# Performance work log

Hardware: AMD Instinct MI355X
Metric: run time of the kernel (lower is better)

The kernel has to match this reference:

```python
import jax, jax.numpy as jnp
import numpy as np

S = 2048          # sequence length (single prefill sequence)
HID = 4096        # hidden_size
NH, NKV, HD = 32, 8, 128   # q heads, kv heads, head_dim
THETA = 10000.0
SCALE = HD ** -0.5


def setup_inputs() -> dict:
    key = jax.random.key(0)
    k1, k2, k3 = jax.random.split(key, 3)
    hidden_states = jax.random.normal(k1, (S, HID), jnp.float32)
    positions = jnp.arange(S, dtype=jnp.int32)
    W_qkv = jax.random.normal(k2, (HID, (NH + 2 * NKV) * HD), jnp.float32) * 0.02
    W_o = jax.random.normal(k3, (NH * HD, HID), jnp.float32) * 0.02
    return {"hidden_states": hidden_states, "positions": positions,
            "W_qkv": W_qkv, "W_o": W_o}


def _rope(x, positions):
    # x: [T, H, HD]; neox-style RoPE (rotate halves, is_neox_style=True)
    half = HD // 2
    inv_freq = 1.0 / (THETA ** (jnp.arange(half, dtype=jnp.float32) / half))
    freqs = positions.astype(jnp.float32)[:, None] * inv_freq[None, :]  # [T, half]
    cos = jnp.cos(freqs)[:, None, :]
    sin = jnp.sin(freqs)[:, None, :]
    x1, x2 = x[..., :half], x[..., half:]
    return jnp.concatenate([x1 * cos - x2 * sin, x2 * cos + x1 * sin], axis=-1)


def reference(hidden_states, positions, W_qkv, W_o):
    # fused QKV projection then split (q_size = NH*HD, kv_size = NKV*HD)
    qkv = hidden_states @ W_qkv                      # [S, (NH+2*NKV)*HD]
    q, k, v = jnp.split(qkv, [NH * HD, NH * HD + NKV * HD], axis=1)
    q = _rope(q.reshape(S, NH, HD), positions)       # [S, NH, HD]
    k = _rope(k.reshape(S, NKV, HD), positions)      # [S, NKV, HD]
    v = v.reshape(S, NKV, HD)
    # GQA: broadcast kv heads to query heads
    rep = NH // NKV
    k = jnp.repeat(k, rep, axis=1)                   # [S, NH, HD]
    v = jnp.repeat(v, rep, axis=1)
    scores = jnp.einsum('qhd,khd->hqk', q, k) * SCALE  # [NH, S, S]
    causal = jnp.tril(jnp.ones((S, S), dtype=bool))
    scores = jnp.where(causal[None], scores, jnp.finfo(scores.dtype).min)
    attn = jax.nn.softmax(scores, axis=-1)
    out = jnp.einsum('hqk,khd->qhd', attn, v).reshape(S, NH * HD)
    return out @ W_o                                 # [S, HID]
```

## Files before the change

kernel.cpp:

```cpp
#include <hip/hip_runtime.h>
#include <math.h>

#define S_LEN 2048
#define HID 4096
#define NH 32
#define NKV 8
#define HD 128
#define QKV_N ((NH + 2*NKV) * HD)
#define NQK (NH + NKV)
static __device__ __constant__ const float SCALE_F = 0.08838834764831845f;

typedef __bf16 bf16x8 __attribute__((ext_vector_type(8)));
typedef __bf16 bf16x4 __attribute__((ext_vector_type(4)));
typedef float  f32x4  __attribute__((ext_vector_type(4)));

#define GLD_LDS(gptr, lptr) \
  __builtin_amdgcn_global_load_lds( \
      (const __attribute__((address_space(1))) uint32_t*)(gptr), \
      (__attribute__((address_space(3))) uint32_t*)(lptr), 16, 0, 0)

__global__ void cast_bf16_kernel(const float4* __restrict__ in, __bf16* __restrict__ out, int n4) {
  int i = blockIdx.x * blockDim.x + threadIdx.x;
  if (i >= n4) return;
  float4 v = in[i];
  bf16x4 o = { (__bf16)v.x, (__bf16)v.y, (__bf16)v.z, (__bf16)v.w };
  *(bf16x4*)(out + (size_t)i * 4) = o;
}

__global__ void transpose_cast_kernel(const float* __restrict__ in, __bf16* __restrict__ out,
                                      int R, int C) {
  __shared__ float tile[32][33];
  int bx = blockIdx.x * 32;
  int by = blockIdx.y * 32;
  int tx = threadIdx.x, ty = threadIdx.y;
  for (int i = 0; i < 32; i += 8)
    tile[ty + i][tx] = in[(size_t)(by + ty + i) * C + bx + tx];
  __syncthreads();
  for (int i = 0; i < 32; i += 8)
    out[(size_t)(bx + ty + i) * R + by + tx] = (__bf16)tile[tx][ty + i];
}

__global__ void transpose_v_kernel(const __bf16* __restrict__ qkv, __bf16* __restrict__ Vt) {
  __shared__ __bf16 tile[32][33];
  int kvh = blockIdx.z;
  int sb = blockIdx.x * 32;
  int db = blockIdx.y * 32;
  int tx = threadIdx.x, ty = threadIdx.y;
  const __bf16* src = qkv + (size_t)(NH + NKV) * HD + (size_t)kvh * HD;
  for (int i = 0; i < 32; i += 8)
    tile[ty + i][tx] = src[(size_t)(sb + ty + i) * QKV_N + db + tx];
  __syncthreads();
  for (int i = 0; i < 32; i += 8)
    Vt[((size_t)kvh * HD + db + ty + i) * S_LEN + sb + tx] = tile[tx][ty + i];
}

__global__ void rope_kernel(const __bf16* __restrict__ qkv, const int* __restrict__ pos,
                            __bf16* __restrict__ Qr, __bf16* __restrict__ Kr) {
  int idx = blockIdx.x * blockDim.x + threadIdx.x;
  int half = idx & 63;
  int t = idx >> 6;
  int hh = t % NQK;
  int s = t / NQK;
  if (s >= S_LEN) return;
  float p = (float)pos[s];
  float inv_freq = exp2f((float)half * -0.2076205059304601f);
  float ang = p * inv_freq;
  float cs = cosf(ang), sn = sinf(ang);
  const __bf16* src; __bf16* dst;
  if (hh < NH) {
    src = qkv + (size_t)s * QKV_N + (size_t)hh * HD;
    dst = Qr + ((size_t)s * NH + hh) * HD;
  } else {
    int kh = hh - NH;
    src = qkv + (size_t)s * QKV_N + (size_t)NH * HD + (size_t)kh * HD;
    dst = Kr + ((size_t)s * NKV + kh) * HD;
  }
  float x1 = (float)src[half], x2 = (float)src[half + 64];
  dst[half]      = (__bf16)(x1 * cs - x2 * sn);
  dst[half + 64] = (__bf16)(x2 * cs + x1 * sn);
}

template <typename OutT>
__global__ __launch_bounds__(512, 2) void gemm8p_kernel(const __bf16* __restrict__ A,
                                                        const __bf16* __restrict__ Bt,
                                                        OutT* __restrict__ C,
                                                        int M, int N, int K) {
  __shared__ __align__(16) __bf16 sA[2][2][256 * 32];
  __shared__ __align__(16) __bf16 sB[2][2][256 * 32];
  const int tid = threadIdx.x;
  const int lane = tid & 63;
  const int wave = tid >> 6;
  const int quad = lane >> 4;
  const int l16 = lane & 15;
  const int wm = (wave >> 2) * 128;
  const int wn = (wave & 3) * 64;
  const size_t bm = (size_t)blockIdx.y * 256;
  const size_t bn = (size_t)blockIdx.x * 256;
  const int NT = K >> 6;
  const int rsw = (l16 >> 1) & 3;

  f32x4 acc[8][4] = {};
  bf16x8 aR[4], bR[4];

#define STAGE(gbase, rowbase, tau, h, dst) do {                                   \
    size_t kof_ = (size_t)((tau) % NT) * 64 + (h) * 32;                           \
    _Pragma("unroll")                                                             \
    for (int it_ = 0; it_ < 2; ++it_) {                                           \
      int c_ = it_ * 512 + tid;                                                   \
      int row_ = c_ >> 2, ch_ = c_ & 3;                                           \
      int chL_ = ch_ ^ ((row_ >> 1) & 3);                                         \
      GLD_LDS(&(gbase)[((rowbase) + row_) * (size_t)K + kof_ + chL_ * 8],         \
              &(dst)[c_ * 8]);                                                    \
    }                                                                             \
  } while (0)

#define LOADB(bf, kk) do {                                                        \
    _Pragma("unroll")                                                             \
    for (int j_ = 0; j_ < 4; ++j_)                                                \
      bR[j_] = *(const bf16x8*)&sB[bf][kk][(wn + j_ * 16 + l16) * 32 +            \
                                           ((quad ^ rsw) * 8)];                   \
  } while (0)

#define LOADA(bf, kk, ih) do {                                                    \
    _Pragma("unroll")                                                             \
    for (int i_ = 0; i_ < 4; ++i_)                                                \
      aR[i_] = *(const bf16x8*)&sA[bf][kk][(wm + ((ih) * 4 + i_) * 16 + l16) * 32 \
                                           + ((quad ^ rsw) * 8)];                 \
  } while (0)

#define MFMA16(ih) do {                                                           \
    __builtin_amdgcn_s_setprio(1);                                                \
    _Pragma("unroll")                                                             \
    for (int i_ = 0; i_ < 4; ++i_)                                                \
      _Pragma("unroll")                                                           \
      for (int j_ = 0; j_ < 4; ++j_)                                              \
        acc[(ih) * 4 + i_][j_] = __builtin_amdgcn_mfma_f32_16x16x32_bf16(         \
            aR[i_], bR[j_], acc[(ih) * 4 + i_][j_], 0, 0, 0);                     \
    __builtin_amdgcn_s_setprio(0);                                                \
  } while (0)

#define BAR() __builtin_amdgcn_s_barrier()
#define VMCNT4() asm volatile("s_waitcnt vmcnt(4)" ::: "memory")

  STAGE(A,  bm, 0, 0, sA[0][0]);
  STAGE(Bt, bn, 0, 0, sB[0][0]);
  STAGE(A,  bm, 0, 1, sA[0][1]);
  STAGE(Bt, bn, 0, 1, sB[0][1]);
  STAGE(A,  bm, 1, 0, sA[1][0]);
  STAGE(Bt, bn, 1, 0, sB[1][0]);
  VMCNT4();
  BAR();

  for (int u = 0; u < (NT >> 1); ++u) {
    const int t0 = 2 * u;
    LOADB(0, 0); LOADA(0, 0, 0);
    STAGE(A, bm, t0 + 1, 1, sA[1][1]);
    BAR();
    MFMA16(0);
    BAR();
    LOADA(0, 0, 1);
    STAGE(Bt, bn, t0 + 1, 1, sB[1][1]);
    BAR();
    MFMA16(1);
    BAR();
    LOADB(0, 1); LOADA(0, 1, 0);
    STAGE(A, bm, t0 + 2, 0, sA[0][0]);
    BAR();
    MFMA16(0);
    BAR();
    LOADA(0, 1, 1);
    STAGE(Bt, bn, t0 + 2, 0, sB[0][0]);
    BAR();
    MFMA16(1);
    VMCNT4();
    BAR();
    LOADB(1, 0); LOADA(1, 0, 0);
    STAGE(A, bm, t0 + 2, 1, sA[0][1]);
    BAR();
    MFMA16(0);
    BAR();
    LOADA(1, 0, 1);
    STAGE(Bt, bn, t0 + 2, 1, sB[0][1]);
    BAR();
    MFMA16(1);
    BAR();
    LOADB(1, 1); LOADA(1, 1, 0);
    STAGE(A, bm, t0 + 3, 0, sA[1][0]);
    BAR();
    MFMA16(0);
    BAR();
    LOADA(1, 1, 1);
    STAGE(Bt, bn, t0 + 3, 0, sB[1][0]);
    BAR();
    MFMA16(1);
    VMCNT4();
    BAR();
  }

  asm volatile("s_waitcnt vmcnt(0)" ::: "memory");

  #pragma unroll
  for (int i = 0; i < 8; ++i)
    #pragma unroll
    for (int j = 0; j < 4; ++j)
      #pragma unroll
      for (int r = 0; r < 4; ++r) {
        size_t row = bm + wm + i * 16 + quad * 4 + r;
        size_t col = bn + wn + j * 16 + l16;
        C[row * (size_t)N + col] = (OutT)acc[i][j][r];
      }

#undef STAGE
#undef LOADB
#undef LOADA
#undef MFMA16
#undef BAR
#undef VMCNT4
}

__global__ __launch_bounds__(256, 2) void attn_kernel(const __bf16* __restrict__ Qr,
                                                      const __bf16* __restrict__ Kr,
                                                      const __bf16* __restrict__ Vt,
                                                      __bf16* __restrict__ O) {
  __shared__ __align__(16) char smem[73728];
  __bf16* Ps = (__bf16*)(smem + 65536);

  const int bid = blockIdx.x;
  const int h = bid & (NH - 1);
  const int qb = (S_LEN / 64 - 1) - (bid >> 5);
  const int kvh = h >> 2;
  const int tid = threadIdx.x;
  const int lane = tid & 63, wave = tid >> 6;
  const int quad = lane >> 4, l16 = lane & 15;
  const int sw = l16 & 7;
  const int q0 = qb * 64;

#define STAGE_KV(kbase, bufv) do {                                                 \
    char* kd_ = smem + (bufv) * 16384;                                             \
    char* vd_ = smem + 32768 + (bufv) * 16384;                                     \
    _Pragma("unroll")                                                              \
    for (int pass_ = 0; pass_ < 4; ++pass_) {                                      \
      int c_ = pass_ * 256 + tid;                                                  \
      int row_ = c_ >> 4, ch_ = c_ & 15;                                           \
      int chs_ = ch_ ^ (row_ & 7);                                                 \
      GLD_LDS(&Kr[(size_t)((kbase) + row_) * (NKV * HD) + (size_t)kvh * HD + chs_ * 8], \
              kd_ + c_ * 16);                                                      \
    }                                                                              \
    _Pragma("unroll")                                                              \
    for (int pass_ = 0; pass_ < 4; ++pass_) {                                      \
      int c_ = pass_ * 256 + tid;                                                  \
      int d_ = c_ >> 3, ch_ = c_ & 7;                                              \
      int chs_ = ch_ ^ (d_ & 7);                                                   \
      GLD_LDS(&Vt[((size_t)kvh * HD + d_) * S_LEN + (kbase) + chs_ * 8],           \
              vd_ + c_ * 16);                                                      \
    }                                                                              \
  } while (0)

  bf16x8 qf[4];
  {
    const __bf16* qp = Qr + (size_t)(q0 + wave * 16 + l16) * (NH * HD) + (size_t)h * HD + quad * 8;
    for (int kk = 0; kk < 4; ++kk) qf[kk] = *(const bf16x8*)(qp + kk * 32);
  }
  f32x4 oacc[8] = {};
  float m2 = -INFINITY, l_i = 0.0f;
  const float C2 = SCALE_F * 1.4426950408889634f;

  int buf = 0;
  STAGE_KV(0, 0);
  for (int kb = 0; kb <= q0; kb += 64) {
    __syncthreads();
    if (kb + 64 <= q0) STAGE_KV(kb + 64, buf ^ 1);

    const __bf16* Ks = (const __bf16*)(smem + buf * 16384);
    const __bf16* Vs = (const __bf16*)(smem + 32768 + buf * 16384);

    f32x4 sc[4] = {};
    __builtin_amdgcn_s_setprio(1);
    for (int jt = 0; jt < 4; ++jt)
      for (int kk = 0; kk < 4; ++kk) {
        bf16x8 kf = *(const bf16x8*)&Ks[(jt * 16 + l16) * 128 + ((kk * 4 + quad) ^ sw) * 8];
        sc[jt] = __builtin_amdgcn_mfma_f32_16x16x32_bf16(kf, qf[kk], sc[jt], 0, 0, 0);
      }
    __builtin_amdgcn_s_setprio(0);

    float s[16];
    for (int jt = 0; jt < 4; ++jt)
      for (int r = 0; r < 4; ++r) s[jt * 4 + r] = sc[jt][r];
    if (kb == q0) {
      int qloc = wave * 16 + l16;
      for (int jt = 0; jt < 4; ++jt)
        for (int r = 0; r < 4; ++r)
          if (jt * 16 + quad * 4 + r > qloc) s[jt * 4 + r] = -INFINITY;
    }
    float mx = s[0];
    for (int i = 1; i < 16; ++i) mx = fmaxf(mx, s[i]);
    mx = fmaxf(mx, __shfl_xor(mx, 16, 64));
    mx = fmaxf(mx, __shfl_xor(mx, 32, 64));
    float m2new = fmaxf(m2, mx * C2);
    float alpha = exp2f(m2 - m2new);
    float pv[16], sum = 0.0f;
    for (int i = 0; i < 16; ++i) { pv[i] = exp2f(fmaf(s[i], C2, -m2new)); sum += pv[i]; }
    sum += __shfl_xor(sum, 16, 64);
    sum += __shfl_xor(sum, 32, 64);
    l_i = l_i * alpha + sum;
    m2 = m2new;
    for (int dt = 0; dt < 8; ++dt) oacc[dt] *= alpha;

    __bf16* pw = Ps + wave * 1024 + l16 * 64;
    for (int jt = 0; jt < 4; ++jt) {
      bf16x4 pk = { (__bf16)pv[jt*4+0], (__bf16)pv[jt*4+1], (__bf16)pv[jt*4+2], (__bf16)pv[jt*4+3] };
      int chunk = jt * 2 + (quad >> 1);
      *(bf16x4*)&pw[((chunk ^ sw) * 8) + (quad & 1) * 4] = pk;
    }
    __builtin_amdgcn_s_setprio(1);
    for (int half = 0; half < 2; ++half) {
      bf16x8 pf = *(const bf16x8*)&pw[((half * 4 + quad) ^ sw) * 8];
      for (int dt = 0; dt < 8; ++dt) {
        bf16x8 vf = *(const bf16x8*)&Vs[(dt * 16 + l16) * 64 + ((half * 4 + quad) ^ sw) * 8];
        oacc[dt] = __builtin_amdgcn_mfma_f32_16x16x32_bf16(vf, pf, oacc[dt], 0, 0, 0);
      }
    }
    __builtin_amdgcn_s_setprio(0);
    buf ^= 1;
  }
  __syncthreads();

#undef STAGE_KV

  float* scr = (float*)smem + wave * 2112;
  float inv = 1.0f / l_i;
  for (int dt = 0; dt < 8; ++dt) {
    f32x4 v = oacc[dt] * inv;
    *(f32x4*)&scr[l16 * 132 + dt * 16 + quad * 4] = v;
  }
  for (int it = 0; it < 4; ++it) {
    int c = it * 64 + lane;
    int row = c >> 4, ch = c & 15;
    const float* sp = &scr[row * 132 + ch * 8];
    f32x4 a = *(const f32x4*)sp;
    f32x4 b = *(const f32x4*)(sp + 4);
    bf16x8 o = { (__bf16)a[0], (__bf16)a[1], (__bf16)a[2], (__bf16)a[3],
                 (__bf16)b[0], (__bf16)b[1], (__bf16)b[2], (__bf16)b[3] };
    *(bf16x8*)&O[(size_t)(q0 + wave * 16 + row) * (NH * HD) + (size_t)h * HD + ch * 8] = o;
  }
}

extern "C" void kernel_launch(void* const* d_in, const int* in_sizes, int n_in,
                              void* d_out, int out_size, void* d_ws, size_t ws_size,
                              hipStream_t stream) {
  const float* hidden    = (const float*)d_in[0];
  const int*   positions = (const int*)d_in[1];
  const float* Wqkv      = (const float*)d_in[2];
  const float* Wo        = (const float*)d_in[3];
  float* out = (float*)d_out;

  char* p = (char*)d_ws;
  auto alloc = [&](size_t bytes) { char* r = p; p += (bytes + 255) & ~(size_t)255; return r; };
  __bf16* hid_bf = (__bf16*)alloc((size_t)S_LEN * HID * 2);
  __bf16* wqkvT  = (__bf16*)alloc((size_t)QKV_N * HID * 2);
  __bf16* woT    = (__bf16*)alloc((size_t)HID * HID * 2);
  __bf16* qkv    = (__bf16*)alloc((size_t)S_LEN * QKV_N * 2);
  __bf16* Qr     = (__bf16*)alloc((size_t)S_LEN * NH * HD * 2);
  __bf16* Kr     = (__bf16*)alloc((size_t)S_LEN * NKV * HD * 2);
  __bf16* Vt     = (__bf16*)alloc((size_t)S_LEN * NKV * HD * 2);
  __bf16* attn   = hid_bf;

  {
    int n4 = S_LEN * HID / 4;
    cast_bf16_kernel<<<(n4 + 255) / 256, 256, 0, stream>>>((const float4*)hidden, hid_bf, n4);
  }
  transpose_cast_kernel<<<dim3(QKV_N / 32, HID / 32), dim3(32, 8), 0, stream>>>(Wqkv, wqkvT, HID, QKV_N);
  transpose_cast_kernel<<<dim3(HID / 32, HID / 32), dim3(32, 8), 0, stream>>>(Wo, woT, HID, HID);
  gemm8p_kernel<__bf16><<<dim3(QKV_N / 256, S_LEN / 256), 512, 0, stream>>>(
      hid_bf, wqkvT, qkv, S_LEN, QKV_N, HID);
  {
    int total = S_LEN * NQK * 64;
    rope_kernel<<<total / 256, 256, 0, stream>>>(qkv, positions, Qr, Kr);
  }
  transpose_v_kernel<<<dim3(S_LEN / 32, HD / 32, NKV), dim3(32, 8), 0, stream>>>(qkv, Vt);
  attn_kernel<<<NH * (S_LEN / 64), 256, 0, stream>>>(Qr, Kr, Vt, attn);
  gemm8p_kernel<float><<<dim3(HID / 256, S_LEN / 256), 512, 0, stream>>>(
      attn, woT, out, S_LEN, HID, HID);
}
```

Before: 560.9 us.

## Swizzle GEMM block order and hand-schedule LDS reads with inline asm

Remaps the GEMM workgroup index with an XCD-aware swizzle so neighbouring tiles run on the same chiplet and share L2. Replaces the compiler-generated LDS fragment loads with inline ds_read_b128 using immediate offsets from a precomputed base address. Adds explicit lgkmcnt waits and sched_barriers to pin the order of reads and MFMAs. The manual waits remove the compiler's freedom to overlap LDS reads with MFMA work, and the swizzle assumes the workgroup count is a multiple of 8.

```diff
diff --git a/kernel.cpp b/kernel.cpp
--- a/kernel.cpp
+++ b/kernel.cpp
@@ -1,5 +1,6 @@
 #include <hip/hip_runtime.h>
 #include <math.h>
+#include <stdint.h>
 
 #define S_LEN 2048
 #define HID 4096
@@ -13,6 +14,7 @@
 typedef __bf16 bf16x8 __attribute__((ext_vector_type(8)));
 typedef __bf16 bf16x4 __attribute__((ext_vector_type(4)));
 typedef float  f32x4  __attribute__((ext_vector_type(4)));
+typedef uint32_t u32x4 __attribute__((ext_vector_type(4)));
 
 #define GLD_LDS(gptr, lptr) \
   __builtin_amdgcn_global_load_lds( \
@@ -94,13 +96,42 @@
   const int l16 = lane & 15;
   const int wm = (wave >> 2) * 128;
   const int wn = (wave & 3) * 64;
-  const size_t bm = (size_t)blockIdx.y * 256;
-  const size_t bn = (size_t)blockIdx.x * 256;
+
+  const int nx = gridDim.x;
+  const int nwg = nx * gridDim.y;
+  int bid = blockIdx.y * nx + blockIdx.x;
+  int swz = (bid & 7) * (nwg >> 3) + (bid >> 3);
+  const size_t bm = (size_t)(swz / nx) * 256;
+  const size_t bn = (size_t)(swz % nx) * 256;
+
   const int NT = K >> 6;
   const int rsw = (l16 >> 1) & 3;
 
   f32x4 acc[8][4] = {};
   bf16x8 aR[4], bR[4];
+
+  typedef __attribute__((address_space(3))) __bf16 lds_bf16;
+  const uint32_t sAb = (uint32_t)(uintptr_t)(lds_bf16*)&sA[0][0][0];
+  const uint32_t sBb = (uint32_t)(uintptr_t)(lds_bf16*)&sB[0][0][0];
+  const uint32_t aBase = sAb + (uint32_t)(((wm + l16) * 32 + (quad ^ rsw) * 8) * 2);
+  const uint32_t bBase = sBb + (uint32_t)(((wn + l16) * 32 + (quad ^ rsw) * 8) * 2);
+
+#define DSRD4(dst, baseaddr) do {                                                 \
+    u32x4 t0_, t1_, t2_, t3_;                                                     \
+    asm volatile("ds_read_b128 %0, %4\n\t"                                        \
+                 "ds_read_b128 %1, %4 offset:1024\n\t"                            \
+                 "ds_read_b128 %2, %4 offset:2048\n\t"                            \
+                 "ds_read_b128 %3, %4 offset:3072"                                \
+                 : "=&v"(t0_), "=&v"(t1_), "=&v"(t2_), "=&v"(t3_)                 \
+                 : "v"(baseaddr));                                                \
+    dst[0] = __builtin_bit_cast(bf16x8, t0_);                                     \
+    dst[1] = __builtin_bit_cast(bf16x8, t1_);                                     \
+    dst[2] = __builtin_bit_cast(bf16x8, t2_);                                     \
+    dst[3] = __builtin_bit_cast(bf16x8, t3_);                                     \
+  } while (0)
+
+#define LOADB(bf, kk) DSRD4(bR, bBase + (bf) * 32768u + (kk) * 16384u)
+#define LOADA(bf, kk, ih) DSRD4(aR, aBase + (bf) * 32768u + (kk) * 16384u + (ih) * 4096u)
 
 #define STAGE(gbase, rowbase, tau, h, dst) do {                                   \
     size_t kof_ = (size_t)((tau) % NT) * 64 + (h) * 32;                           \
@@ -114,20 +145,6 @@
     }                                                                             \
   } while (0)
 
-#define LOADB(bf, kk) do {                                                        \
-    _Pragma("unroll")                                                             \
-    for (int j_ = 0; j_ < 4; ++j_)                                                \
-      bR[j_] = *(const bf16x8*)&sB[bf][kk][(wn + j_ * 16 + l16) * 32 +            \
-                                           ((quad ^ rsw) * 8)];                   \
-  } while (0)
-
-#define LOADA(bf, kk, ih) do {                                                    \
-    _Pragma("unroll")                                                             \
-    for (int i_ = 0; i_ < 4; ++i_)                                                \
-      aR[i_] = *(const bf16x8*)&sA[bf][kk][(wm + ((ih) * 4 + i_) * 16 + l16) * 32 \
-                                           + ((quad ^ rsw) * 8)];                 \
-  } while (0)
-
 #define MFMA16(ih) do {                                                           \
     __builtin_amdgcn_s_setprio(1);                                                \
     _Pragma("unroll")                                                             \
@@ -137,9 +154,12 @@
         acc[(ih) * 4 + i_][j_] = __builtin_amdgcn_mfma_f32_16x16x32_bf16(         \
             aR[i_], bR[j_], acc[(ih) * 4 + i_][j_], 0, 0, 0);                     \
     __builtin_amdgcn_s_setprio(0);                                                \
+    __builtin_amdgcn_sched_barrier(0);                                            \
   } while (0)
 
 #define BAR() __builtin_amdgcn_s_barrier()
+#define LGKM0() do { asm volatile("s_waitcnt lgkmcnt(0)");                        \
+                     __builtin_amdgcn_sched_barrier(0); } while (0)
 #define VMCNT4() asm volatile("s_waitcnt vmcnt(4)" ::: "memory")
 
   STAGE(A,  bm, 0, 0, sA[0][0]);
@@ -156,42 +176,50 @@
     LOADB(0, 0); LOADA(0, 0, 0);
     STAGE(A, bm, t0 + 1, 1, sA[1][1]);
     BAR();
+    LGKM0();
     MFMA16(0);
     BAR();
     LOADA(0, 0, 1);
     STAGE(Bt, bn, t0 + 1, 1, sB[1][1]);
     BAR();
+    LGKM0();
     MFMA16(1);
     BAR();
     LOADB(0, 1); LOADA(0, 1, 0);
     STAGE(A, bm, t0 + 2, 0, sA[0][0]);
     BAR();
+    LGKM0();
     MFMA16(0);
     BAR();
     LOADA(0, 1, 1);
     STAGE(Bt, bn, t0 + 2, 0, sB[0][0]);
     BAR();
+    LGKM0();
     MFMA16(1);
     VMCNT4();
     BAR();
     LOADB(1, 0); LOADA(1, 0, 0);
     STAGE(A, bm, t0 + 2, 1, sA[0][1]);
     BAR();
+    LGKM0();
     MFMA16(0);
     BAR();
     LOADA(1, 0, 1);
     STAGE(Bt, bn, t0 + 2, 1, sB[0][1]);
     BAR();
+    LGKM0();
     MFMA16(1);
     BAR();
     LOADB(1, 1); LOADA(1, 1, 0);
     STAGE(A, bm, t0 + 3, 0, sA[1][0]);
     BAR();
+    LGKM0();
     MFMA16(0);
     BAR();
     LOADA(1, 1, 1);
     STAGE(Bt, bn, t0 + 3, 0, sB[1][0]);
     BAR();
+    LGKM0();
     MFMA16(1);
     VMCNT4();
     BAR();
@@ -213,8 +241,10 @@
 #undef STAGE
 #undef LOADB
 #undef LOADA
+#undef DSRD4
 #undef MFMA16
 #undef BAR
+#undef LGKM0
 #undef VMCNT4
 }
 
```

After: 539.7 us. 1.04x faster.
